# Kernel optimization log

Hardware: AMD Instinct MI355X
Metric: run time of the kernel (lower is better)

Reference implementation:

```python
import jax, jax.numpy as jnp
import numpy as np

EPS = 1e-7          # keras backend epsilon
BN_EPS = 1e-3       # keras BatchNormalization default epsilon
SCALES = (2, 4, 8, 16, 32)  # 2**i for i in 1..max_scale, max_scale=5


def _box_filter(x, k):
    # depthwise conv with all-ones k x k kernel, SAME padding (TF semantics)
    c = x.shape[-1]
    kern = jnp.ones((k, k, 1, c), x.dtype)
    return jax.lax.conv_general_dilated(
        x, kern, (1, 1), 'SAME',
        dimension_numbers=('NHWC', 'HWIO', 'NHWC'),
        feature_group_count=c)


def setup_inputs() -> dict:
    key = jax.random.key(0)
    ks = jax.random.split(key, 4)
    B, H, W, C, R = 16, 56, 56, 128, 8
    x = jax.random.normal(ks[0], (B, H, W, C), jnp.float32)
    kappa = jax.random.uniform(ks[1], (len(SCALES),), jnp.float32, -0.5, 0.5)
    W1 = jax.random.normal(ks[2], (C, C // R), jnp.float32) * (1.0 / np.sqrt(C))
    b1 = jnp.zeros((C // R,), jnp.float32)
    W2 = jax.random.normal(ks[3], (C // R, C), jnp.float32) * (1.0 / np.sqrt(C // R))
    b2 = jnp.zeros((C,), jnp.float32)
    gamma = jnp.ones((C,), jnp.float32)
    beta = jnp.zeros((C,), jnp.float32)
    bn_mean = jnp.zeros((C,), jnp.float32)
    bn_var = jnp.ones((C,), jnp.float32)
    return dict(x=x, kappa=kappa, W1=W1, b1=b1, W2=W2, b2=b2,
                gamma=gamma, beta=beta, bn_mean=bn_mean, bn_var=bn_var)


def reference(x, kappa, W1, b1, W2, b2, gamma, beta, bn_mean, bn_var):
    # per-sample min-max scaling over (H, W, C)
    xmin = jnp.min(x, axis=(1, 2, 3), keepdims=True)
    xmax = jnp.max(x, axis=(1, 2, 3), keepdims=True)
    xs = (x - xmin) / (xmax - xmin + EPS)

    # multi-scale box measures: [B,H,W,C,S]
    measures = jnp.stack([_box_filter(xs, k) for k in SCALES], axis=-1)
    log_m = jnp.log(measures + EPS)
    log_r = jnp.log(jnp.asarray(SCALES, jnp.float32))  # [S]

    # OLS slope of log_m vs log_r along scale axis -> alphas [B,H,W,C]
    xc = log_r - jnp.mean(log_r)
    alphas = jnp.sum(log_m * xc, axis=-1) / jnp.sum(xc * xc)

    # squeeze-and-excite on alphas
    squeeze = jnp.mean(alphas, axis=(1, 2))            # [B,C]
    hidden = jax.nn.relu(squeeze @ W1 + b1)            # [B,C//r]
    excite = jax.nn.sigmoid(hidden @ W2 + b2)          # [B,C]

    # weighted OLS estimate: alpha * (log_k + log_r) -> [B,H,W,C,S]
    k_ = jax.nn.sigmoid(kappa)
    log_k = jax.nn.sigmoid(jnp.log(k_ + EPS))          # [S]
    wols = alphas[..., None] * (log_k + log_r)

    # standardized (mean-centered) cosine similarity along scale axis, in [0,1]
    a = log_m - jnp.mean(log_m, axis=-1, keepdims=True)
    b = wols - jnp.mean(wols, axis=-1, keepdims=True)
    cos = jnp.sum(a * b, axis=-1) / (
        jnp.linalg.norm(a, axis=-1) * jnp.linalg.norm(b, axis=-1) + EPS)
    sim = 0.5 * (cos + 1.0)                            # [B,H,W,C]

    # inference-mode batchnorm on alphas
    alpha_norm = gamma * (alphas - bn_mean) * jax.lax.rsqrt(bn_var + BN_EPS) + beta

    x_exc = xs * excite[:, None, None, :]
    return sim * jax.nn.sigmoid(alpha_norm) + (1.0 - sim) * x_exc
```

## Files before the change

kernel.cpp:

```cpp
#include <hip/hip_runtime.h>
#include <hip/hip_fp16.h>

#define NTOT   6422528
#define NPERB  401408
#define NQ     100352
#define LOG2E  1.4426950408889634f

__device__ __forceinline__ float sigmoidf_fast(float x) {
    return __builtin_amdgcn_rcpf(1.f + __expf(-x));
}

__device__ __forceinline__ unsigned encf(float f) {
    unsigned u = __float_as_uint(f);
    return (u & 0x80000000u) ? ~u : (u | 0x80000000u);
}
__device__ __forceinline__ float decf(unsigned u) {
    return __uint_as_float((u & 0x80000000u) ? (u ^ 0x80000000u) : ~u);
}

__device__ __forceinline__ void kappa_consts(const float* kap, float* dcs) {
    float v[5]; float mean = 0.f;
    for (int s = 0; s < 5; s++) {
        float lr = 0.6931471805599453f * (float)(s + 1);
        float k_ = 1.f / (1.f + expf(-kap[s]));
        float lk = 1.f / (1.f + expf(-logf(k_ + 1e-7f)));
        v[s] = lk + lr; mean += v[s];
    }
    mean *= 0.2f; float nd = 0.f;
    for (int s = 0; s < 5; s++) { float d = v[s] - mean; dcs[s] = d; nd += d * d; }
    dcs[5] = sqrtf(nd);
}

struct ScaleU { int rb1, rb0; float xmch; };

__global__ void k_minmax(const float4* __restrict__ x4,
                         unsigned* __restrict__ pmnu, unsigned* __restrict__ pmxu) {
    int p = blockIdx.x;
    int b = p & 15, chunk = p >> 4;
    const float4* base = x4 + b * NQ + chunk * 3136;
    float mn = 3.4e38f, mx = -3.4e38f;
    for (int q = threadIdx.x; q < 3136; q += 256) {
        float4 v = base[q];
        mn = fminf(mn, fminf(fminf(v.x, v.y), fminf(v.z, v.w)));
        mx = fmaxf(mx, fmaxf(fmaxf(v.x, v.y), fmaxf(v.z, v.w)));
    }
    __shared__ float rmn[256], rmx[256];
    int tid = threadIdx.x;
    rmn[tid] = mn; rmx[tid] = mx;
    __syncthreads();
    for (int s = 128; s > 0; s >>= 1) {
        if (tid < s) {
            rmn[tid] = fminf(rmn[tid], rmn[tid + s]);
            rmx[tid] = fmaxf(rmx[tid], rmx[tid + s]);
        }
        __syncthreads();
    }
    if (tid == 0) {
        atomicMin(&pmnu[b], encf(rmn[0]));
        atomicMax(&pmxu[b], encf(rmx[0]));
    }
}

__launch_bounds__(1024)
__global__ void k_satg(const float* __restrict__ x,   const float* __restrict__ kap,
                       const float* __restrict__ gam, const float* __restrict__ bet,
                       const float* __restrict__ bnm, const float* __restrict__ bnv,
                       const unsigned* __restrict__ pmnu, const unsigned* __restrict__ pmxu,
                       float* __restrict__ sq, unsigned int* __restrict__ ABu) {
    __shared__ float SATl[57 * 57 * 8];
    __shared__ float tot[448];
    __shared__ float wsum[112];
    __shared__ float cst[9];

    const int p = blockIdx.x;
    const int b = p & 15, cg = p >> 4;
    const int c0 = cg * 8;
    const int tid = threadIdx.x;
    const int seg = (tid >= 448) ? 1 : 0;
    const int idx = tid - seg * 448;
    const int cc = idx & 7, lj = idx >> 3;
    const bool act = (tid < 896);

    for (int z = tid; z < 456; z += 1024) SATl[z] = 0.f;
    for (int z = tid; z < 456; z += 1024) SATl[(z >> 3) * 456 + (z & 7)] = 0.f;

    float v[28];
    if (act) {
        const float* xp = x + b * NPERB + (seg * 28) * 7168 + lj * 128 + c0 + cc;
        float acc = 0.f;
#pragma unroll
        for (int k = 0; k < 28; k++) { acc += xp[k * 7168]; v[k] = acc; }
        if (seg == 0) {
#pragma unroll
            for (int k = 0; k < 28; k++) SATl[(k + 1) * 456 + (lj + 1) * 8 + cc] = v[k];
            tot[idx] = acc;
        }
    }
    __syncthreads();
    if (act && seg == 1) {
        float basev = tot[idx];
#pragma unroll
        for (int k = 0; k < 28; k++) SATl[(k + 29) * 456 + (lj + 1) * 8 + cc] = basev + v[k];
    }
    if (tid == 896) {
        float d[6]; kappa_consts(kap, d);
        for (int s2 = 0; s2 < 6; s2++) cst[s2] = d[s2];
    } else if (tid == 897) {
        float mnv = decf(pmnu[b]), mxv = decf(pmxu[b]);
        float xi = 1.f / (mxv - mnv + 1e-7f);
        cst[6] = mnv; cst[7] = xi; cst[8] = mnv * xi;
    }
    __syncthreads();

    if (act) {
        const int colbase = (lj + 1) * 456 + cc;
#pragma unroll
        for (int k = 0; k < 28; k++) v[k] = SATl[colbase + (seg * 28 + 1 + k) * 8];
#pragma unroll
        for (int k = 1; k < 28; k++) v[k] += v[k - 1];
        if (seg == 0) {
#pragma unroll
            for (int k = 0; k < 28; k++) SATl[colbase + (1 + k) * 8] = v[k];
            tot[idx] = v[27];
        }
    }
    __syncthreads();
    if (act && seg == 1) {
        const int colbase = (lj + 1) * 456 + cc;
        float basev = tot[idx];
#pragma unroll
        for (int k = 0; k < 28; k++) SATl[colbase + (29 + k) * 8] = basev + v[k];
    }
    __syncthreads();

    float asum = 0.f;
    if (act) {
        const int i = lj;
        const int j0 = seg * 28;
        const float xm = cst[6], xi = cst[7], xmxi = cst[8];
        const int ci = c0 + cc;
        const float g = gam[ci], be = bet[ci], bm = bnm[ci];
        const float rsv = rsqrtf(bnv[ci] + 1e-3f);
        const float A1c = g * rsv, A0c = be - g * bm * rsv;
        const float C1 = -A1c * (LOG2E * 0.1f);
        const float C0 = -A0c * LOG2E;
        const float d0 = cst[0], d1 = cst[1], d2 = cst[2], d3 = cst[3], d4 = cst[4], nd = cst[5];
        const float* sp = SATl + cc;

        auto mkU = [&](int hk) {
            ScaleU uu;
            int y1g = min(i + hk, 55) + 1;
            int y0g = max(i - hk + 1, 0);
            uu.rb1 = y1g * 456; uu.rb0 = y0g * 456;
            uu.xmch = xm * (float)(y1g - y0g);
            return uu;
        };
        const ScaleU u0 = mkU(1), u1 = mkU(2), u2 = mkU(4), u3 = mkU(8), u4 = mkU(16);

        auto meas = [&](int j, const ScaleU& uu, int hk) -> float {
            int x1g = min(j + hk, 55) + 1;
            int x0g = max(j - hk + 1, 0);
            float cw = (float)(x1g - x0g);
            int o1 = x1g << 3, o0 = x0g << 3;
            float s = sp[uu.rb1 + o1] - sp[uu.rb0 + o1] - sp[uu.rb1 + o0] + sp[uu.rb0 + o0];
            return __log2f(fmaxf((s - uu.xmch * cw) * xi, 0.f) + 1e-7f);
        };

        const float* xrow = x + b * NPERB + i * 7168 + c0 + cc;
        unsigned int* abrow = ABu + b * NPERB + i * 7168 + c0 + cc;
        for (int jj = 0; jj < 28; jj++) {
            int j = j0 + jj;
            float l0 = meas(j, u0, 1);
            float l1 = meas(j, u1, 2);
            float l2 = meas(j, u2, 4);
            float l3 = meas(j, u3, 8);
            float l4 = meas(j, u4, 16);
            float w2 = -2.f * l0 - l1 + l3 + 2.f * l4;
            asum += w2;
            float alphas = w2 * 0.1f;
            float mean = 0.2f * (l0 + l1 + l2 + l3 + l4);
            float a0 = l0 - mean, a1 = l1 - mean, a2 = l2 - mean, a3 = l3 - mean, a4 = l4 - mean;
            float na2  = a0 * a0 + a1 * a1 + a2 * a2 + a3 * a3 + a4 * a4;
            float adot = a0 * d0 + a1 * d1 + a2 * d2 + a3 * d3 + a4 * d4;
            float na = __builtin_amdgcn_sqrtf(na2);
            float cosv = (alphas * adot) * __builtin_amdgcn_rcpf(na * fabsf(alphas) * nd + 1e-7f);
            float sim = 0.5f * (cosv + 1.f);
            float sbn = __builtin_amdgcn_rcpf(1.f + exp2f(C1 * w2 + C0));
            float xs = fmaf(xrow[j * 128], xi, -xmxi);
            float A = sim * sbn;
            float B = (1.f - sim) * xs;
            abrow[j * 128] = __builtin_bit_cast(unsigned int, __floats2half2_rn(A, B));
        }
    }
    asum += __shfl_down(asum, 32);
    asum += __shfl_down(asum, 16);
    asum += __shfl_down(asum, 8);
    {
        int w = tid >> 6, l = tid & 63;
        if (w < 14 && l < 8) wsum[w * 8 + l] = asum;
    }
    __syncthreads();
    if (tid < 8) {
        float s = 0.f;
#pragma unroll
        for (int w = 0; w < 14; w++) s += wsum[w * 8 + tid];
        atomicAdd(&sq[b * 128 + c0 + tid], s * 0.1f);
    }
}

__launch_bounds__(256)
__global__ void k_mix2(const unsigned int* __restrict__ ABu, const float* __restrict__ sq,
                       const float* __restrict__ W1, const float* __restrict__ b1,
                       const float* __restrict__ W2, const float* __restrict__ b2,
                       float* __restrict__ out) {
    __shared__ float sqz[128];
    __shared__ float hid[16];
    __shared__ float exc[128];
    int p = blockIdx.x;
    int b = p & 15, chunk = p >> 4;
    int tid = threadIdx.x;
    if (tid < 128) sqz[tid] = sq[b * 128 + tid] * (1.f / 3136.f);
    __syncthreads();
    if (tid < 16) {
        float acc = b1[tid];
        for (int c2 = 0; c2 < 128; c2++) acc += sqz[c2] * W1[c2 * 16 + tid];
        hid[tid] = fmaxf(acc, 0.f);
    }
    __syncthreads();
    if (tid < 128) {
        float acc = b2[tid];
#pragma unroll
        for (int h = 0; h < 16; h++) acc += hid[h] * W2[h * 128 + tid];
        exc[tid] = sigmoidf_fast(acc);
    }
    __syncthreads();
    const uint4* ab4 = (const uint4*)ABu;
    float4* out4 = (float4*)out;
    const int base = b * NQ + chunk * 1568;
    for (int q = tid; q < 1568; q += 256) {
        int g = base + q;
        int cb = (g & 31) << 2;
        uint4 u = ab4[g];
        float2 p0 = __half22float2(__builtin_bit_cast(__half2, u.x));
        float2 p1 = __half22float2(__builtin_bit_cast(__half2, u.y));
        float2 p2 = __half22float2(__builtin_bit_cast(__half2, u.z));
        float2 p3 = __half22float2(__builtin_bit_cast(__half2, u.w));
        out4[g] = make_float4(p0.x + p0.y * exc[cb],
                              p1.x + p1.y * exc[cb + 1],
                              p2.x + p2.y * exc[cb + 2],
                              p3.x + p3.y * exc[cb + 3]);
    }
}

extern "C" void kernel_launch(void* const* d_in, const int* in_sizes, int n_in,
                              void* d_out, int out_size, void* d_ws, size_t ws_size,
                              hipStream_t stream) {
    const float* x   = (const float*)d_in[0];
    const float* kap = (const float*)d_in[1];
    const float* W1  = (const float*)d_in[2];
    const float* b1  = (const float*)d_in[3];
    const float* W2  = (const float*)d_in[4];
    const float* b2  = (const float*)d_in[5];
    const float* gam = (const float*)d_in[6];
    const float* bet = (const float*)d_in[7];
    const float* bnm = (const float*)d_in[8];
    const float* bnv = (const float*)d_in[9];
    float* out = (float*)d_out;

    float*    sq   = (float*)d_ws;
    unsigned* pmnu = (unsigned*)(sq + 2048);
    unsigned* pmxu = pmnu + 16;
    unsigned* ABu  = (unsigned*)(pmxu + 16);

    hipMemsetAsync(sq, 0, 2048 * sizeof(float), stream);
    hipMemsetAsync(pmnu, 0xFF, 16 * sizeof(unsigned), stream);
    hipMemsetAsync(pmxu, 0x00, 16 * sizeof(unsigned), stream);

    k_minmax<<<512, 256, 0, stream>>>((const float4*)x, pmnu, pmxu);
    k_satg<<<256, 1024, 0, stream>>>(x, kap, gam, bet, bnm, bnv, pmnu, pmxu, sq, ABu);
    k_mix2<<<1024, 256, 0, stream>>>(ABu, sq, W1, b1, W2, b2, out);
}
```

Baseline: 149.8 us.

## Fuse SE/mix stage into SAT kernel via last-block-per-batch, narrow channel tiles

The separate mix kernel is removed. Its squeeze-excite and output-combine work now runs inside the SAT kernel, in whichever block per batch finishes last, detected with an atomic counter. The SAT kernel now handles 4 channels per block with 896 threads (512 blocks) instead of 8 channels with 1024 threads, giving more blocks and a smaller LDS footprint. The minmax kernel computes min as the max of negated values so a single zero memset initialises all workspace, and it reduces with wave shuffles. The risk is that the whole output write for each batch is left to a single block per batch, which serialises a bandwidth-heavy tail onto only 16 CUs.

Result: slower. 294.0 us (+96.3%).

```diff
diff --git a/kernel.cpp b/kernel.cpp
--- a/kernel.cpp
+++ b/kernel.cpp
@@ -3,7 +3,8 @@
 
 #define NTOT   6422528
 #define NPERB  401408
-#define NQ     100352
+#define NQ4    100352
+#define SATR   228
 #define LOG2E  1.4426950408889634f
 
 __device__ __forceinline__ float sigmoidf_fast(float x) {
@@ -34,109 +35,120 @@
 struct ScaleU { int rb1, rb0; float xmch; };
 
 __global__ void k_minmax(const float4* __restrict__ x4,
-                         unsigned* __restrict__ pmnu, unsigned* __restrict__ pmxu) {
+                         unsigned* __restrict__ pmxu, unsigned* __restrict__ pmnn) {
     int p = blockIdx.x;
     int b = p & 15, chunk = p >> 4;
-    const float4* base = x4 + b * NQ + chunk * 3136;
-    float mn = 3.4e38f, mx = -3.4e38f;
+    const float4* base = x4 + b * NQ4 + chunk * 3136;
+    float mx = -3.4e38f, mn = -3.4e38f;
     for (int q = threadIdx.x; q < 3136; q += 256) {
         float4 v = base[q];
-        mn = fminf(mn, fminf(fminf(v.x, v.y), fminf(v.z, v.w)));
         mx = fmaxf(mx, fmaxf(fmaxf(v.x, v.y), fmaxf(v.z, v.w)));
-    }
-    __shared__ float rmn[256], rmx[256];
-    int tid = threadIdx.x;
-    rmn[tid] = mn; rmx[tid] = mx;
-    __syncthreads();
-    for (int s = 128; s > 0; s >>= 1) {
-        if (tid < s) {
-            rmn[tid] = fminf(rmn[tid], rmn[tid + s]);
-            rmx[tid] = fmaxf(rmx[tid], rmx[tid + s]);
-        }
-        __syncthreads();
-    }
-    if (tid == 0) {
-        atomicMin(&pmnu[b], encf(rmn[0]));
-        atomicMax(&pmxu[b], encf(rmx[0]));
-    }
-}
-
-__launch_bounds__(1024)
+        mn = fmaxf(mn, fmaxf(fmaxf(-v.x, -v.y), fmaxf(-v.z, -v.w)));
+    }
+    __shared__ float rmx[4], rmn[4];
+    int lane = threadIdx.x & 63, w = threadIdx.x >> 6;
+#pragma unroll
+    for (int off = 32; off; off >>= 1) {
+        mx = fmaxf(mx, __shfl_down(mx, off));
+        mn = fmaxf(mn, __shfl_down(mn, off));
+    }
+    if (lane == 0) { rmx[w] = mx; rmn[w] = mn; }
+    __syncthreads();
+    if (threadIdx.x == 0) {
+        mx = fmaxf(fmaxf(rmx[0], rmx[1]), fmaxf(rmx[2], rmx[3]));
+        mn = fmaxf(fmaxf(rmn[0], rmn[1]), fmaxf(rmn[2], rmn[3]));
+        atomicMax(&pmxu[b], encf(mx));
+        atomicMax(&pmnn[b], encf(mn));
+    }
+}
+
+__launch_bounds__(896, 7)
 __global__ void k_satg(const float* __restrict__ x,   const float* __restrict__ kap,
                        const float* __restrict__ gam, const float* __restrict__ bet,
                        const float* __restrict__ bnm, const float* __restrict__ bnv,
-                       const unsigned* __restrict__ pmnu, const unsigned* __restrict__ pmxu,
-                       float* __restrict__ sq, unsigned int* __restrict__ ABu) {
-    __shared__ float SATl[57 * 57 * 8];
-    __shared__ float tot[448];
-    __shared__ float wsum[112];
+                       const unsigned* __restrict__ pmxu, const unsigned* __restrict__ pmnn,
+                       float* __restrict__ sq, unsigned* __restrict__ cnt,
+                       unsigned int* __restrict__ ABu,
+                       const float* __restrict__ W1, const float* __restrict__ b1,
+                       const float* __restrict__ W2, const float* __restrict__ b2,
+                       float* __restrict__ out) {
+    __shared__ float SATl[57 * SATR];
+    __shared__ float tot[896];
+    __shared__ float wsum[56];
     __shared__ float cst[9];
+    __shared__ float sqz[128], hidl[16], excl[128];
+    __shared__ int lastflag;
 
     const int p = blockIdx.x;
     const int b = p & 15, cg = p >> 4;
-    const int c0 = cg * 8;
-    const int tid = threadIdx.x;
-    const int seg = (tid >= 448) ? 1 : 0;
-    const int idx = tid - seg * 448;
-    const int cc = idx & 7, lj = idx >> 3;
-    const bool act = (tid < 896);
-
-    for (int z = tid; z < 456; z += 1024) SATl[z] = 0.f;
-    for (int z = tid; z < 456; z += 1024) SATl[(z >> 3) * 456 + (z & 7)] = 0.f;
-
-    float v[28];
-    if (act) {
-        const float* xp = x + b * NPERB + (seg * 28) * 7168 + lj * 128 + c0 + cc;
-        float acc = 0.f;
-#pragma unroll
-        for (int k = 0; k < 28; k++) { acc += xp[k * 7168]; v[k] = acc; }
-        if (seg == 0) {
-#pragma unroll
-            for (int k = 0; k < 28; k++) SATl[(k + 1) * 456 + (lj + 1) * 8 + cc] = v[k];
-            tot[idx] = acc;
-        }
-    }
-    __syncthreads();
-    if (act && seg == 1) {
-        float basev = tot[idx];
-#pragma unroll
-        for (int k = 0; k < 28; k++) SATl[(k + 29) * 456 + (lj + 1) * 8 + cc] = basev + v[k];
-    }
-    if (tid == 896) {
-        float d[6]; kappa_consts(kap, d);
-        for (int s2 = 0; s2 < 6; s2++) cst[s2] = d[s2];
-    } else if (tid == 897) {
-        float mnv = decf(pmnu[b]), mxv = decf(pmxu[b]);
+    const int c0 = cg * 4;
+    const int t = threadIdx.x;
+    const int cc = t & 3;
+    const int jrow = (t % 224) >> 2;
+    const int seg = t / 224;
+
+    if (t < 228) {
+        SATl[t] = 0.f;
+        SATl[(t >> 2) * SATR + (t & 3)] = 0.f;
+    }
+    if (t == 0) {
+        float mxv = decf(pmxu[b]);
+        float mnv = -decf(pmnn[b]);
         float xi = 1.f / (mxv - mnv + 1e-7f);
         cst[6] = mnv; cst[7] = xi; cst[8] = mnv * xi;
-    }
-    __syncthreads();
-
-    if (act) {
-        const int colbase = (lj + 1) * 456 + cc;
-#pragma unroll
-        for (int k = 0; k < 28; k++) v[k] = SATl[colbase + (seg * 28 + 1 + k) * 8];
-#pragma unroll
-        for (int k = 1; k < 28; k++) v[k] += v[k - 1];
-        if (seg == 0) {
-#pragma unroll
-            for (int k = 0; k < 28; k++) SATl[colbase + (1 + k) * 8] = v[k];
-            tot[idx] = v[27];
-        }
-    }
-    __syncthreads();
-    if (act && seg == 1) {
-        const int colbase = (lj + 1) * 456 + cc;
-        float basev = tot[idx];
-#pragma unroll
-        for (int k = 0; k < 28; k++) SATl[colbase + (29 + k) * 8] = basev + v[k];
+    } else if (t == 64) {
+        float d[6]; kappa_consts(kap, d);
+#pragma unroll
+        for (int s2 = 0; s2 < 6; s2++) cst[s2] = d[s2];
+    }
+
+    float v[14];
+    {
+        const float* xp = x + b * NPERB + (seg * 14) * 7168 + jrow * 128 + c0 + cc;
+        float acc = 0.f;
+#pragma unroll
+        for (int k = 0; k < 14; k++) { acc += xp[k * 7168]; v[k] = acc; }
+        tot[t] = acc;
+    }
+    __syncthreads();
+    {
+        const int tj = jrow * 4 + cc;
+        float base = 0.f;
+        if (seg > 0) base += tot[tj];
+        if (seg > 1) base += tot[224 + tj];
+        if (seg > 2) base += tot[448 + tj];
+#pragma unroll
+        for (int k = 0; k < 14; k++)
+            SATl[(seg * 14 + k + 1) * SATR + (jrow + 1) * 4 + cc] = base + v[k];
+    }
+    __syncthreads();
+
+    {
+        const int colbase = (jrow + 1) * SATR + cc;
+#pragma unroll
+        for (int k = 0; k < 14; k++) v[k] = SATl[colbase + (seg * 14 + 1 + k) * 4];
+#pragma unroll
+        for (int k = 1; k < 14; k++) v[k] += v[k - 1];
+        tot[t] = v[13];
+    }
+    __syncthreads();
+    {
+        const int tj = jrow * 4 + cc;
+        float base = 0.f;
+        if (seg > 0) base += tot[tj];
+        if (seg > 1) base += tot[224 + tj];
+        if (seg > 2) base += tot[448 + tj];
+        const int colbase = (jrow + 1) * SATR + cc;
+#pragma unroll
+        for (int k = 0; k < 14; k++)
+            SATl[colbase + (seg * 14 + 1 + k) * 4] = base + v[k];
     }
     __syncthreads();
 
     float asum = 0.f;
-    if (act) {
-        const int i = lj;
-        const int j0 = seg * 28;
+    {
+        const int i = jrow;
+        const int j0 = seg * 14;
         const float xm = cst[6], xi = cst[7], xmxi = cst[8];
         const int ci = c0 + cc;
         const float g = gam[ci], be = bet[ci], bm = bnm[ci];
@@ -151,7 +163,7 @@
             ScaleU uu;
             int y1g = min(i + hk, 55) + 1;
             int y0g = max(i - hk + 1, 0);
-            uu.rb1 = y1g * 456; uu.rb0 = y0g * 456;
+            uu.rb1 = y1g * SATR; uu.rb0 = y0g * SATR;
             uu.xmch = xm * (float)(y1g - y0g);
             return uu;
         };
@@ -161,14 +173,14 @@
             int x1g = min(j + hk, 55) + 1;
             int x0g = max(j - hk + 1, 0);
             float cw = (float)(x1g - x0g);
-            int o1 = x1g << 3, o0 = x0g << 3;
+            int o1 = x1g << 2, o0 = x0g << 2;
             float s = sp[uu.rb1 + o1] - sp[uu.rb0 + o1] - sp[uu.rb1 + o0] + sp[uu.rb0 + o0];
             return __log2f(fmaxf((s - uu.xmch * cw) * xi, 0.f) + 1e-7f);
         };
 
-        const float* xrow = x + b * NPERB + i * 7168 + c0 + cc;
-        unsigned int* abrow = ABu + b * NPERB + i * 7168 + c0 + cc;
-        for (int jj = 0; jj < 28; jj++) {
+        const float* xrow = x + b * NPERB + i * 7168 + ci;
+        unsigned int* abrow = ABu + b * NPERB + i * 7168 + ci;
+        for (int jj = 0; jj < 14; jj++) {
             int j = j0 + jj;
             float l0 = meas(j, u0, 1);
             float l1 = meas(j, u1, 2);
@@ -195,60 +207,51 @@
     asum += __shfl_down(asum, 32);
     asum += __shfl_down(asum, 16);
     asum += __shfl_down(asum, 8);
-    {
-        int w = tid >> 6, l = tid & 63;
-        if (w < 14 && l < 8) wsum[w * 8 + l] = asum;
-    }
-    __syncthreads();
-    if (tid < 8) {
+    asum += __shfl_down(asum, 4);
+    if ((t & 63) < 4) wsum[(t >> 6) * 4 + (t & 3)] = asum;
+    __syncthreads();
+    if (t < 4) {
         float s = 0.f;
 #pragma unroll
-        for (int w = 0; w < 14; w++) s += wsum[w * 8 + tid];
-        atomicAdd(&sq[b * 128 + c0 + tid], s * 0.1f);
-    }
-}
-
-__launch_bounds__(256)
-__global__ void k_mix2(const unsigned int* __restrict__ ABu, const float* __restrict__ sq,
-                       const float* __restrict__ W1, const float* __restrict__ b1,
-                       const float* __restrict__ W2, const float* __restrict__ b2,
-                       float* __restrict__ out) {
-    __shared__ float sqz[128];
-    __shared__ float hid[16];
-    __shared__ float exc[128];
-    int p = blockIdx.x;
-    int b = p & 15, chunk = p >> 4;
-    int tid = threadIdx.x;
-    if (tid < 128) sqz[tid] = sq[b * 128 + tid] * (1.f / 3136.f);
-    __syncthreads();
-    if (tid < 16) {
-        float acc = b1[tid];
-        for (int c2 = 0; c2 < 128; c2++) acc += sqz[c2] * W1[c2 * 16 + tid];
-        hid[tid] = fmaxf(acc, 0.f);
-    }
-    __syncthreads();
-    if (tid < 128) {
-        float acc = b2[tid];
-#pragma unroll
-        for (int h = 0; h < 16; h++) acc += hid[h] * W2[h * 128 + tid];
-        exc[tid] = sigmoidf_fast(acc);
-    }
-    __syncthreads();
-    const uint4* ab4 = (const uint4*)ABu;
-    float4* out4 = (float4*)out;
-    const int base = b * NQ + chunk * 1568;
-    for (int q = tid; q < 1568; q += 256) {
-        int g = base + q;
-        int cb = (g & 31) << 2;
-        uint4 u = ab4[g];
+        for (int w = 0; w < 14; w++) s += wsum[w * 4 + t];
+        atomicAdd(&sq[b * 128 + c0 + t], s * 0.1f);
+    }
+
+    __threadfence();
+    if (t == 0) lastflag = (atomicAdd(&cnt[b], 1u) == 31u) ? 1 : 0;
+    __syncthreads();
+    if (!lastflag) return;
+    __threadfence();
+
+    if (t < 128) sqz[t] = sq[b * 128 + t] * (1.f / 3136.f);
+    __syncthreads();
+    if (t < 16) {
+        float acc = b1[t];
+        for (int c2 = 0; c2 < 128; c2++) acc += sqz[c2] * W1[c2 * 16 + t];
+        hidl[t] = fmaxf(acc, 0.f);
+    }
+    __syncthreads();
+    if (t < 128) {
+        float acc = b2[t];
+#pragma unroll
+        for (int h = 0; h < 16; h++) acc += hidl[h] * W2[h * 128 + t];
+        excl[t] = sigmoidf_fast(acc);
+    }
+    __syncthreads();
+
+    const uint4* ab4 = (const uint4*)ABu + b * NQ4;
+    float4* out4 = (float4*)out + b * NQ4;
+    for (int q = t; q < NQ4; q += 896) {
+        int cb = (q & 31) << 2;
+        uint4 u = ab4[q];
         float2 p0 = __half22float2(__builtin_bit_cast(__half2, u.x));
         float2 p1 = __half22float2(__builtin_bit_cast(__half2, u.y));
         float2 p2 = __half22float2(__builtin_bit_cast(__half2, u.z));
         float2 p3 = __half22float2(__builtin_bit_cast(__half2, u.w));
-        out4[g] = make_float4(p0.x + p0.y * exc[cb],
-                              p1.x + p1.y * exc[cb + 1],
-                              p2.x + p2.y * exc[cb + 2],
-                              p3.x + p3.y * exc[cb + 3]);
+        out4[q] = make_float4(p0.x + p0.y * excl[cb],
+                              p1.x + p1.y * excl[cb + 1],
+                              p2.x + p2.y * excl[cb + 2],
+                              p3.x + p3.y * excl[cb + 3]);
     }
 }
 
@@ -268,15 +271,13 @@
     float* out = (float*)d_out;
 
     float*    sq   = (float*)d_ws;
-    unsigned* pmnu = (unsigned*)(sq + 2048);
-    unsigned* pmxu = pmnu + 16;
-    unsigned* ABu  = (unsigned*)(pmxu + 16);
-
-    hipMemsetAsync(sq, 0, 2048 * sizeof(float), stream);
-    hipMemsetAsync(pmnu, 0xFF, 16 * sizeof(unsigned), stream);
-    hipMemsetAsync(pmxu, 0x00, 16 * sizeof(unsigned), stream);
-
-    k_minmax<<<512, 256, 0, stream>>>((const float4*)x, pmnu, pmxu);
-    k_satg<<<256, 1024, 0, stream>>>(x, kap, gam, bet, bnm, bnv, pmnu, pmxu, sq, ABu);
-    k_mix2<<<1024, 256, 0, stream>>>(ABu, sq, W1, b1, W2, b2, out);
-}
+    unsigned* pmxu = (unsigned*)(sq + 2048);
+    unsigned* pmnn = pmxu + 16;
+    unsigned* cnt  = pmnn + 16;
+    unsigned* ABu  = (unsigned*)(sq + 2112);
+
+    hipMemsetAsync(d_ws, 0, 8448, stream);
+    k_minmax<<<512, 256, 0, stream>>>((const float4*)x, pmxu, pmnn);
+    k_satg<<<512, 896, 0, stream>>>(x, kap, gam, bet, bnm, bnv, pmxu, pmnn,
+                                    sq, cnt, ABu, W1, b1, W2, b2, out);
+}
```
